# Kernel optimization log

Hardware: AMD Instinct MI355X
Metric: run time of the kernel (lower is better)

The kernel has to match this reference:

```python
import jax, jax.numpy as jnp
import numpy as np

# Static config matching init_kwargs / input_specs
IN_CH = 256
PATCH = 64
LAYERS = 4
B, H, W = 4, 256, 256
IC = IN_CH // 4        # SelfAttention inner channels (reduce=4)
C16 = IN_CH // 16      # f_test conv output channels
ALPHA = 0.05


def conv1x1(x, w, b):
    # x: (b,c,h,w), w: (out,c), b: (out,)  == nn.Conv2d(c,out,1)
    return jnp.einsum('bchw,oc->bohw', x, w) + b[None, :, None, None]


def setup_inputs() -> dict:
    key = jax.random.key(0)
    ks = jax.random.split(key, 12)
    s = 0.05
    return {
        'x':  jax.random.normal(ks[0], (B, IN_CH, H, W), jnp.float32),
        'Wq': jax.random.normal(ks[1], (IC, IN_CH), jnp.float32) * s,
        'bq': jax.random.normal(ks[2], (IC,), jnp.float32) * s,
        'Wk': jax.random.normal(ks[3], (IC, IN_CH), jnp.float32) * s,
        'bk': jax.random.normal(ks[4], (IC,), jnp.float32) * s,
        'Wv': jax.random.normal(ks[5], (IC, IN_CH), jnp.float32) * s,
        'bv': jax.random.normal(ks[6], (IC,), jnp.float32) * s,
        'Wr': jax.random.normal(ks[7], (IN_CH, IC), jnp.float32) * s,
        'br': jax.random.normal(ks[8], (IN_CH,), jnp.float32) * s,
        'Wf': jax.random.normal(ks[9], (C16, IN_CH), jnp.float32) * s,
        'bf': jax.random.normal(ks[10], (C16,), jnp.float32) * s,
    }


def reference(x, Wq, bq, Wk, bk, Wv, bv, Wr, br, Wf, bf):
    b, c, h, w = x.shape
    p = PATCH
    nh = h // p
    ic = IC

    # f_test applies the same 1x1 conv to the FULL image every call; its output
    # is identical each time, so precompute the per-(batch,channel) mean/var once.
    # torch uses .detach() -> stop_gradient.
    y2 = jax.lax.stop_gradient(conv1x1(x, Wf, bf))           # (b, C16, h, w)
    m2 = y2.mean(axis=(2, 3))                                 # (b, C16)
    v2 = y2.var(axis=(2, 3))                                  # biased var
    n1 = float(p * p)
    n2 = float(h * w)
    dfw = n1 + n2 - 2.0

    def ftest_decision(patch):
        # Two-group one-way ANOVA (scipy.stats.f_oneway) per (batch, channel).
        y1 = jax.lax.stop_gradient(conv1x1(patch, Wf, bf))    # (b, C16, p, p)
        m1 = y1.mean(axis=(2, 3))
        v1 = y1.var(axis=(2, 3))
        gm = (n1 * m1 + n2 * m2) / (n1 + n2)
        ssb = n1 * (m1 - gm) ** 2 + n2 * (m2 - gm) ** 2       # df_between = 1
        ssw = n1 * v1 + n2 * v2                               # sum sq dev within
        Fst = ssb / (ssw / dfw)
        # p-value = sf of F(1, dfw) = I_{dfw/(dfw+F)}(dfw/2, 1/2)
        pval = jax.scipy.special.betainc(dfw / 2.0, 0.5, dfw / (dfw + Fst))
        counts = jnp.sum(pval < ALPHA)
        return counts * 2 >= m1.size                          # scalar bool

    def attn(patch):
        # SelfAttention.forward: channel-to-channel attention over a patch.
        Q = conv1x1(patch, Wq, bq).reshape(b, ic, p * p)      # (b, ic, pp)
        # NOTE: original does K_pro.view(b, -1, inner_ch) -- a raw reshape,
        # NOT a transpose; we reproduce that exactly.
        K = conv1x1(patch, Wk, bk).reshape(b, p * p, ic)      # (b, pp, ic)
        V = conv1x1(patch, Wv, bv).reshape(b, ic, p * p)
        wts = jax.nn.softmax(jnp.einsum('bim,bmj->bij', Q, K), axis=1)  # (b,ic,ic)
        att = jnp.einsum('bij,bjm->bim', wts, V).reshape(b, ic, p, p)
        return conv1x1(att, Wr, br) + patch

    def run_patch(patch):
        # layer loop with data-dependent early break, expressed via masking
        stopped = jnp.array(False)
        for _ in range(LAYERS):
            stopped = stopped | ftest_decision(patch)  # break BEFORE attention
            patch = jnp.where(stopped, patch, attn(patch))
        return patch

    # Extract all nh*nh patches: (n_patches, b, c, p, p)
    patches = (x.reshape(b, c, nh, p, nh, p)
                .transpose(2, 4, 0, 1, 3, 5)
                .reshape(nh * nh, b, c, p, p))
    out_patches = jax.vmap(run_patch)(patches)

    # Faithful to original bug: x1 = x.clone() happens inside the patch loop,
    # so only the LAST patch's update survives in the returned tensor.
    x1 = x.at[:, :, (nh - 1) * p:, (nh - 1) * p:].set(out_patches[-1])
    return x1
```

## Files before the change

kernel.cpp:

```cpp
#include <hip/hip_runtime.h>

#define FCRIT 3.8415923532

#define OFF_FULL   0u
#define OFF_PATCH  1024u
#define OFF_S      8192u
#define OFF_Y3     1048576u
#define OFF_XH     16777216u
#define OFF_WH     41943040u
#define STATS_ZERO_BYTES 270336u

typedef __attribute__((ext_vector_type(8))) short short8;
typedef __attribute__((ext_vector_type(8))) unsigned short us8;
typedef __attribute__((ext_vector_type(4))) float f32x4;

static __device__ __forceinline__ double wred(double v) {
#pragma unroll
  for (int off = 32; off > 0; off >>= 1) v += __shfl_down(v, off, 64);
  return v;
}

static __device__ __forceinline__ unsigned short f2bf(float f) {
  union { float f; unsigned u; } v; v.f = f;
  unsigned r = v.u + 0x7fffu + ((v.u >> 16) & 1u);
  return (unsigned short)(r >> 16);
}
static __device__ __forceinline__ float bf2f(unsigned short h) {
  union { unsigned u; float f; } v; v.u = ((unsigned)h) << 16;
  return v.f;
}

static __device__ __forceinline__ bool is_stopped(const double* __restrict__ fullS,
                                                  const double* __restrict__ patchS,
                                                  int upto) {
  const int k = threadIdx.x & 63;
  const double fs = fullS[2 * k], fq = fullS[2 * k + 1];
  const double m2 = fs * (1.0 / 65536.0);
  const double v2 = fq * (1.0 / 65536.0) - m2 * m2;
  bool stopped = false;
  for (int l = 0; l <= upto; ++l) {
    const double* ps = patchS + (size_t)l * 128;
    const double s1 = ps[2 * k], s2 = ps[2 * k + 1];
    const double m1 = s1 * (1.0 / 4096.0);
    const double v1 = s2 * (1.0 / 4096.0) - m1 * m1;
    const double gm = (4096.0 * m1 + 65536.0 * m2) * (1.0 / 69632.0);
    const double d1 = m1 - gm, d2 = m2 - gm;
    const double ssb = 4096.0 * d1 * d1 + 65536.0 * d2 * d2;
    const double ssw = 4096.0 * v1 + 65536.0 * v2;
    const double F = ssb * (69630.0 / ssw);
    const unsigned long long bal = __ballot(F > FCRIT);
    const int cnt = __popcll(bal);
    stopped = stopped || (2 * cnt >= 64);
  }
  return stopped;
}

static __device__ __forceinline__ void fma16(float acc[4][4], float4 w, float4 v) {
  const float wa[4] = {w.x, w.y, w.z, w.w};
  const float va[4] = {v.x, v.y, v.z, v.w};
#pragma unroll
  for (int a = 0; a < 4; ++a)
#pragma unroll
    for (int c = 0; c < 4; ++c) acc[a][c] += wa[a] * va[c];
}

static __device__ __forceinline__ size_t pidx(int b, int c, int y, int x) {
  return (((size_t)b * 256 + c) * 256 + 192 + y) * 256 + 192 + x;
}

__global__ __launch_bounds__(256) void k_wcvt(const float* __restrict__ Wq,
                                              const float* __restrict__ Wk,
                                              const float* __restrict__ Wv,
                                              unsigned short* __restrict__ Whml) {
  const int idx0 = (blockIdx.x * 256 + threadIdx.x) * 4;
#pragma unroll
  for (int u = 0; u < 4; ++u) {
    const int i = idx0 + u;
    const int row = i >> 8, col = i & 255;
    const float v = (row < 64) ? Wq[row * 256 + col]
                  : (row < 128) ? Wk[(row - 64) * 256 + col]
                                : Wv[(row - 128) * 256 + col];
    const unsigned short h = f2bf(v);
    const float r1 = v - bf2f(h);
    const unsigned short m = f2bf(r1);
    const float r2 = r1 - bf2f(m);
    const unsigned short l = f2bf(r2);
    Whml[i] = h;
    Whml[49152 + i] = m;
    Whml[98304 + i] = l;
  }
}

__global__ __launch_bounds__(256) void k_main(const float* __restrict__ x,
                                              const float* __restrict__ Wf,
                                              const float* __restrict__ bf,
                                              float* __restrict__ out,
                                              double* __restrict__ fullS,
                                              double* __restrict__ patchS0) {
  __shared__ __align__(16) float WfT2[16 * 257];
  __shared__ __align__(16) float WfT[256 * 16];
  __shared__ double sm[4][16][2];
  __shared__ double sp[4][16][2];
  const int t = threadIdx.x;
  const int bb = blockIdx.x >> 7;
  const int rp = blockIdx.x & 127;

  for (int r = 0; r < 16; ++r) {
    int idx = r * 256 + t;
    WfT2[(idx >> 8) * 257 + (idx & 255)] = Wf[idx];
  }
  __syncthreads();
  for (int r = 0; r < 16; ++r) {
    int idx = r * 256 + t;
    int c = idx >> 4, o = idx & 15;
    WfT[c * 16 + o] = WfT2[o * 257 + c];
  }
  __syncthreads();

  const int r0 = rp * 2 + (t >> 7);
  const int col2 = (t & 127) * 2;
  const size_t base = (size_t)bb * 16777216 + (size_t)r0 * 256 + col2;
  const float* xp = x + base;
  float* op = out + base;
  const bool pStore = (rp >= 96) && ((t & 127) >= 96);

  float y0[16], y1[16];
#pragma unroll
  for (int o = 0; o < 16; ++o) { y0[o] = 0.f; y1[o] = 0.f; }

  for (int cb = 0; cb < 32; ++cb) {
    double v[8];
#pragma unroll
    for (int u = 0; u < 8; ++u)
      v[u] = *reinterpret_cast<const double*>(xp + (size_t)(cb * 8 + u) * 65536);
#pragma unroll
    for (int u = 0; u < 8; ++u) {
      double* dst = reinterpret_cast<double*>(op + (size_t)(cb * 8 + u) * 65536);
      if (pStore) *dst = v[u];
      else __builtin_nontemporal_store(v[u], dst);
      const int c = cb * 8 + u;
      float2 f = *reinterpret_cast<const float2*>(&v[u]);
      const float4* wf = reinterpret_cast<const float4*>(&WfT[c * 16]);
      const float4 w0 = wf[0], w1 = wf[1], w2 = wf[2], w3 = wf[3];
      const float wv[16] = {w0.x, w0.y, w0.z, w0.w, w1.x, w1.y, w1.z, w1.w,
                            w2.x, w2.y, w2.z, w2.w, w3.x, w3.y, w3.z, w3.w};
#pragma unroll
      for (int o = 0; o < 16; ++o) {
        y0[o] += wv[o] * f.x;
        y1[o] += wv[o] * f.y;
      }
    }
  }

  const int w = t >> 6, lane = t & 63;
  const bool pBlock = (rp >= 96);
  const bool pLane = ((t & 127) >= 96);
#pragma unroll 1
  for (int o = 0; o < 16; ++o) {
    const float bo = bf[o];
    const double a0 = (double)(y0[o] + bo), a1 = (double)(y1[o] + bo);
    double s1 = a0 + a1, s2 = a0 * a0 + a1 * a1;
    const double r1 = wred(s1), r2 = wred(s2);
    if (lane == 0) { sm[w][o][0] = r1; sm[w][o][1] = r2; }
    if (pBlock) {
      double p1 = pLane ? s1 : 0.0, p2 = pLane ? s2 : 0.0;
      p1 = wred(p1); p2 = wred(p2);
      if (lane == 0) { sp[w][o][0] = p1; sp[w][o][1] = p2; }
    }
  }
  __syncthreads();
  if (t < 32) {
    const int o = t >> 1, wh = t & 1;
    double s = sm[0][o][wh] + sm[1][o][wh] + sm[2][o][wh] + sm[3][o][wh];
    unsafeAtomicAdd(&fullS[(bb * 16 + o) * 2 + wh], s);
    if (pBlock) {
      double p = sp[0][o][wh] + sp[1][o][wh] + sp[2][o][wh] + sp[3][o][wh];
      unsafeAtomicAdd(&patchS0[(bb * 16 + o) * 2 + wh], p);
    }
  }
}

__global__ __launch_bounds__(256) void k_xcvt(const float* __restrict__ out,
                                              unsigned short* __restrict__ Xhml,
                                              const double* __restrict__ fullS,
                                              const double* __restrict__ patchS, int layer) {
  if (is_stopped(fullS, patchS, layer)) return;
  __shared__ float T[256 * 65];
  const int t = threadIdx.x;
  const int bb = blockIdx.x >> 6;
  const int y = blockIdx.x & 63;
  for (int r = 0; r < 64; ++r) {
    int idx = r * 256 + t;
    T[(idx >> 6) * 65 + (idx & 63)] = out[pidx(bb, idx >> 6, y, idx & 63)];
  }
  __syncthreads();
  const int px = t >> 2, c0 = (t & 3) * 64;
  const size_t dstbase = ((size_t)bb * 4096 + y * 64 + px) * 256 + c0;
#pragma unroll 1
  for (int g = 0; g < 8; ++g) {
    us8 hv, mv, lv;
#pragma unroll
    for (int j = 0; j < 8; ++j) {
      const float v = T[(c0 + g * 8 + j) * 65 + px];
      const unsigned short h = f2bf(v);
      const float r1 = v - bf2f(h);
      const unsigned short m = f2bf(r1);
      const float r2 = r1 - bf2f(m);
      const unsigned short l = f2bf(r2);
      hv[j] = (unsigned short)h; mv[j] = m; lv[j] = l;
    }
    *reinterpret_cast<us8*>(Xhml + dstbase + g * 8) = hv;
    *reinterpret_cast<us8*>(Xhml + 4194304u + dstbase + g * 8) = mv;
    *reinterpret_cast<us8*>(Xhml + 8388608u + dstbase + g * 8) = lv;
  }
}

__global__ __launch_bounds__(256) void k_qkv(const unsigned short* __restrict__ Whml,
                                             const float* __restrict__ bq,
                                             const float* __restrict__ bk,
                                             const float* __restrict__ bv,
                                             const unsigned short* __restrict__ Xhml,
                                             float* __restrict__ Y3,
                                             const double* __restrict__ fullS,
                                             const double* __restrict__ patchS, int layer) {
  if (is_stopped(fullS, patchS, layer)) return;
  __shared__ __align__(16) unsigned short Al[3][64][40];
  __shared__ __align__(16) unsigned short Bl[3][128][40];
  const int t = threadIdx.x;
  const int nt = blockIdx.x & 31;
  const int mt = (blockIdx.x >> 5) % 3;
  const int bb = blockIdx.x / 96;
  const int w = t >> 6, lane = t & 63;
  const int lo16 = lane & 15, hi4 = lane >> 4;

  f32x4 acc[4][2];
#pragma unroll
  for (int mf = 0; mf < 4; ++mf)
#pragma unroll
    for (int nf = 0; nf < 2; ++nf) acc[mf][nf] = (f32x4)0.f;

  const unsigned short* Wbase = Whml + mt * 64 * 256;
  const unsigned short* Xbase = Xhml + ((size_t)bb * 4096 + nt * 128) * 256;
  const int am = t >> 2, ak = (t & 3) * 8;
  const int bpx = t >> 1, bkh = (t & 1) * 16;

  for (int kc = 0; kc < 8; ++kc) {
    const int k0 = kc * 32;
    __syncthreads();
#pragma unroll
    for (int lev = 0; lev < 3; ++lev) {
      const us8 va = *reinterpret_cast<const us8*>(Wbase + lev * 49152 + am * 256 + k0 + ak);
      *reinterpret_cast<us8*>(&Al[lev][am][ak]) = va;
      const unsigned short* s = Xbase + (size_t)lev * 4194304 + (size_t)bpx * 256 + k0 + bkh;
      const us8 v0 = *reinterpret_cast<const us8*>(s);
      const us8 v1 = *reinterpret_cast<const us8*>(s + 8);
      *reinterpret_cast<us8*>(&Bl[lev][bpx][bkh]) = v0;
      *reinterpret_cast<us8*>(&Bl[lev][bpx][bkh + 8]) = v1;
    }
    __syncthreads();

    short8 af[3][4], bfr[3][2];
    const int koff = hi4 * 8;
#pragma unroll
    for (int lev = 0; lev < 3; ++lev) {
#pragma unroll
      for (int mf = 0; mf < 4; ++mf)
        af[lev][mf] = *reinterpret_cast<const short8*>(&Al[lev][mf * 16 + lo16][koff]);
#pragma unroll
      for (int nf = 0; nf < 2; ++nf)
        bfr[lev][nf] = *reinterpret_cast<const short8*>(&Bl[lev][w * 32 + nf * 16 + lo16][koff]);
    }
#pragma unroll
    for (int mf = 0; mf < 4; ++mf)
#pragma unroll
      for (int nf = 0; nf < 2; ++nf) {
        f32x4 c = acc[mf][nf];
        c = __builtin_amdgcn_mfma_f32_16x16x32_bf16(af[0][mf], bfr[0][nf], c, 0, 0, 0);
        c = __builtin_amdgcn_mfma_f32_16x16x32_bf16(af[0][mf], bfr[1][nf], c, 0, 0, 0);
        c = __builtin_amdgcn_mfma_f32_16x16x32_bf16(af[1][mf], bfr[0][nf], c, 0, 0, 0);
        c = __builtin_amdgcn_mfma_f32_16x16x32_bf16(af[0][mf], bfr[2][nf], c, 0, 0, 0);
        c = __builtin_amdgcn_mfma_f32_16x16x32_bf16(af[2][mf], bfr[0][nf], c, 0, 0, 0);
        c = __builtin_amdgcn_mfma_f32_16x16x32_bf16(af[1][mf], bfr[1][nf], c, 0, 0, 0);
        acc[mf][nf] = c;
      }
  }

  const float* bias = (mt == 0) ? bq : (mt == 1) ? bk : bv;
#pragma unroll
  for (int mf = 0; mf < 4; ++mf)
#pragma unroll
    for (int nf = 0; nf < 2; ++nf)
#pragma unroll
      for (int r = 0; r < 4; ++r) {
        const int mrow = mf * 16 + hi4 * 4 + r;
        const int col = nt * 128 + w * 32 + nf * 16 + lo16;
        Y3[((size_t)bb * 192 + mt * 64 + mrow) * 4096 + col] = acc[mf][nf][r] + bias[mrow];
      }
}

__global__ __launch_bounds__(256) void k_s(const float* __restrict__ Y3,
                                           float* __restrict__ Sbase,
                                           const double* __restrict__ fullS,
                                           const double* __restrict__ patchS, int layer) {
  if (is_stopped(fullS, patchS, layer)) return;
  __shared__ __align__(16) float QT[64][68];
  __shared__ __align__(16) float K2[64 * 64];
  const int t = threadIdx.x;
  const int mc = blockIdx.x & 63;
  const int bb = blockIdx.x >> 6;
  const int m0 = mc * 64;
  const float* Q = Y3 + (size_t)bb * 192 * 4096;
  const float* Kf = Q + 64 * 4096;
  for (int r = 0; r < 16; ++r) {
    int idx = r * 256 + t;
    int i = idx >> 6, ml = idx & 63;
    QT[ml][i] = Q[(size_t)i * 4096 + m0 + ml];
  }
  for (int r = 0; r < 16; ++r) {
    int idx = r * 256 + t;
    K2[idx] = Kf[(size_t)m0 * 64 + idx];
  }
  __syncthreads();
  const int tj = t & 15, ti = t >> 4;
  float acc[4][4] = {};
#pragma unroll 8
  for (int mm = 0; mm < 64; ++mm) {
    const float4 qv = *reinterpret_cast<const float4*>(&QT[mm][ti * 4]);
    const float4 kv = *reinterpret_cast<const float4*>(&K2[mm * 64 + tj * 4]);
    fma16(acc, qv, kv);
  }
  float* Sl = Sbase + (size_t)layer * 16384 + bb * 4096;
#pragma unroll
  for (int a = 0; a < 4; ++a)
#pragma unroll
    for (int c = 0; c < 4; ++c)
      unsafeAtomicAdd(&Sl[(ti * 4 + a) * 64 + tj * 4 + c], acc[a][c]);
}

__global__ __launch_bounds__(256) void k_awr(const float* __restrict__ Y3,
                                             const float* __restrict__ Sbase,
                                             const float* __restrict__ Wr,
                                             const float* __restrict__ br,
                                             float* __restrict__ out,
                                             const double* __restrict__ fullS,
                                             const double* __restrict__ patchS, int layer) {
  if (is_stopped(fullS, patchS, layer)) return;
  __shared__ __align__(16) float Sw[64 * 68];
  __shared__ __align__(16) float AV[64 * 68];
  __shared__ __align__(16) float WrF[128 * 65];
  const int t = threadIdx.x;
  const int y = blockIdx.x & 63;
  const int oh = (blockIdx.x >> 6) & 1;
  const int bb = blockIdx.x >> 7;

  const float* Vp = Y3 + (size_t)bb * 192 * 4096 + (size_t)128 * 4096 + y * 64;
  for (int r = 0; r < 16; ++r) {
    int idx = r * 256 + t;
    int j = idx >> 6, xx = idx & 63;
    AV[j * 68 + xx] = Vp[(size_t)j * 4096 + xx];
  }
  const float* Sl = Sbase + (size_t)layer * 16384 + bb * 4096;
  for (int r = 0; r < 16; ++r) {
    int idx = r * 256 + t;
    Sw[(idx & 63) * 68 + (idx >> 6)] = Sl[idx];
  }
  for (int r = 0; r < 32; ++r) {
    int idx = r * 256 + t;
    int ol = idx >> 6, i = idx & 63;
    WrF[ol * 65 + i] = Wr[(oh * 128 + ol) * 64 + i];
  }
  __syncthreads();

  if (t < 64) {
    float* colp = &Sw[t * 68];
    float mx = -1e30f;
#pragma unroll
    for (int i = 0; i < 64; ++i) mx = fmaxf(mx, colp[i]);
    float sum = 0.f;
#pragma unroll
    for (int i = 0; i < 64; ++i) {
      float e = __expf(colp[i] - mx);
      colp[i] = e;
      sum += e;
    }
    const float inv = 1.f / sum;
#pragma unroll
    for (int i = 0; i < 64; ++i) colp[i] *= inv;
  }
  __syncthreads();

  {
    const int ti = t >> 4, tx = t & 15;
    float acc[4][4] = {};
#pragma unroll 8
    for (int j = 0; j < 64; ++j) {
      const float4 wv = *reinterpret_cast<const float4*>(&Sw[j * 68 + ti * 4]);
      const float4 vv = *reinterpret_cast<const float4*>(&AV[j * 68 + tx * 4]);
      fma16(acc, wv, vv);
    }
    __syncthreads();
#pragma unroll
    for (int a = 0; a < 4; ++a) {
      float4 res;
      res.x = acc[a][0]; res.y = acc[a][1]; res.z = acc[a][2]; res.w = acc[a][3];
      *reinterpret_cast<float4*>(&AV[(ti * 4 + a) * 68 + tx * 4]) = res;
    }
  }
  __syncthreads();

  const int to = t >> 3, tx8 = t & 7;
  float acc[4][8] = {};
#pragma unroll 4
  for (int i = 0; i < 64; ++i) {
    const float4 a0 = *reinterpret_cast<const float4*>(&AV[i * 68 + tx8 * 8]);
    const float4 a1 = *reinterpret_cast<const float4*>(&AV[i * 68 + tx8 * 8 + 4]);
    const float av[8] = {a0.x, a0.y, a0.z, a0.w, a1.x, a1.y, a1.z, a1.w};
#pragma unroll
    for (int a = 0; a < 4; ++a) {
      const float wv = WrF[(to * 4 + a) * 65 + i];
#pragma unroll
      for (int c = 0; c < 8; ++c) acc[a][c] += wv * av[c];
    }
  }
#pragma unroll
  for (int a = 0; a < 4; ++a) {
    const int o = oh * 128 + to * 4 + a;
    const float bro = br[o];
    float* p = out + pidx(bb, o, y, tx8 * 8);
    float4 p0 = *reinterpret_cast<const float4*>(p);
    float4 p1 = *reinterpret_cast<const float4*>(p + 4);
    p0.x += acc[a][0] + bro; p0.y += acc[a][1] + bro;
    p0.z += acc[a][2] + bro; p0.w += acc[a][3] + bro;
    p1.x += acc[a][4] + bro; p1.y += acc[a][5] + bro;
    p1.z += acc[a][6] + bro; p1.w += acc[a][7] + bro;
    *reinterpret_cast<float4*>(p) = p0;
    *reinterpret_cast<float4*>(p + 4) = p1;
  }
}

__global__ __launch_bounds__(256) void k_ftest(const float* __restrict__ out,
                                               const float* __restrict__ Wf,
                                               const float* __restrict__ bf,
                                               double* __restrict__ patchS,
                                               const double* __restrict__ fullS, int layer) {
  if (is_stopped(fullS, patchS, layer)) return;
  __shared__ __align__(16) float WfT2[16 * 257];
  __shared__ __align__(16) float WfT[256 * 16];
  __shared__ float part[2 * 128 * 17];
  __shared__ double red[16][16][2];
  const int t = threadIdx.x;
  const int bb = blockIdx.x >> 5;
  const int rg = blockIdx.x & 31;

  for (int r = 0; r < 16; ++r) {
    int idx = r * 256 + t;
    WfT2[(idx >> 8) * 257 + (idx & 255)] = Wf[idx];
  }
  __syncthreads();
  for (int r = 0; r < 16; ++r) {
    int idx = r * 256 + t;
    int c = idx >> 4, o = idx & 15;
    WfT[c * 16 + o] = WfT2[o * 257 + c];
  }
  __syncthreads();

  const int h = t >> 7;
  const int px = t & 127;
  const int row = 192 + rg * 2 + (px >> 6);
  const int col = 192 + (px & 63);
  const size_t base = (size_t)bb * 16777216 + (size_t)h * 128 * 65536 + (size_t)row * 256 + col;

  float y[16] = {};
  for (int cb = 0; cb < 16; ++cb) {
    float v[8];
#pragma unroll
    for (int u = 0; u < 8; ++u)
      v[u] = out[base + (size_t)(cb * 8 + u) * 65536];
#pragma unroll
    for (int u = 0; u < 8; ++u) {
      const int c = h * 128 + cb * 8 + u;
      const float4* wf = reinterpret_cast<const float4*>(&WfT[c * 16]);
      const float4 w0 = wf[0], w1 = wf[1], w2 = wf[2], w3 = wf[3];
      const float wv[16] = {w0.x, w0.y, w0.z, w0.w, w1.x, w1.y, w1.z, w1.w,
                            w2.x, w2.y, w2.z, w2.w, w3.x, w3.y, w3.z, w3.w};
#pragma unroll
      for (int o = 0; o < 16; ++o) y[o] += wv[o] * v[u];
    }
  }
#pragma unroll
  for (int o = 0; o < 16; ++o) part[(h * 128 + px) * 17 + o] = y[o];
  __syncthreads();

  const int oo = t & 15, pxg = t >> 4;
  double s1 = 0.0, s2 = 0.0;
  const float bo = bf[oo];
#pragma unroll
  for (int j = 0; j < 8; ++j) {
    const int p = pxg * 8 + j;
    const float yv = part[p * 17 + oo] + part[(128 + p) * 17 + oo] + bo;
    const double v = (double)yv;
    s1 += v;
    s2 += v * v;
  }
  red[oo][pxg][0] = s1;
  red[oo][pxg][1] = s2;
  __syncthreads();
  if (t < 32) {
    const int o = t >> 1, wh = t & 1;
    double s = 0.0;
#pragma unroll
    for (int g = 0; g < 16; ++g) s += red[o][g][wh];
    unsafeAtomicAdd(&patchS[(size_t)(layer + 1) * 128 + (bb * 16 + o) * 2 + wh], s);
  }
}

extern "C" void kernel_launch(void* const* d_in, const int* in_sizes, int n_in,
                              void* d_out, int out_size, void* d_ws, size_t ws_size,
                              hipStream_t stream) {
  const float* x  = (const float*)d_in[0];
  const float* Wq = (const float*)d_in[1];
  const float* bq = (const float*)d_in[2];
  const float* Wk = (const float*)d_in[3];
  const float* bk = (const float*)d_in[4];
  const float* Wv = (const float*)d_in[5];
  const float* bv = (const float*)d_in[6];
  const float* Wr = (const float*)d_in[7];
  const float* br = (const float*)d_in[8];
  const float* Wf = (const float*)d_in[9];
  const float* bf = (const float*)d_in[10];
  float* out = (float*)d_out;
  char* ws = (char*)d_ws;

  double* fullS  = (double*)(ws + OFF_FULL);
  double* patchS = (double*)(ws + OFF_PATCH);
  float* Sb = (float*)(ws + OFF_S);
  float* Y3 = (float*)(ws + OFF_Y3);
  unsigned short* Xhml = (unsigned short*)(ws + OFF_XH);
  unsigned short* Whml = (unsigned short*)(ws + OFF_WH);

  (void)hipMemsetAsync(ws, 0, STATS_ZERO_BYTES, stream);
  k_wcvt<<<48, 256, 0, stream>>>(Wq, Wk, Wv, Whml);
  k_main<<<512, 256, 0, stream>>>(x, Wf, bf, out, fullS, patchS);
  for (int l = 0; l < 4; ++l) {
    k_xcvt<<<256, 256, 0, stream>>>(out, Xhml, fullS, patchS, l);
    k_qkv<<<384, 256, 0, stream>>>(Whml, bq, bk, bv, Xhml, Y3, fullS, patchS, l);
    k_s<<<256, 256, 0, stream>>>(Y3, Sb, fullS, patchS, l);
    k_awr<<<512, 256, 0, stream>>>(Y3, Sb, Wr, br, out, fullS, patchS, l);
    if (l < 3) k_ftest<<<128, 256, 0, stream>>>(out, Wf, bf, patchS, fullS, l);
  }
}
```

Baseline: 252.4 us.

## Compute all layers speculatively, fuse bf16 split into producers, select result at end

Drops the per-kernel stop checks and computes all four attention layers unconditionally. Each layer's result goes to a pixel-major buffer, and a final selection kernel copies the correct layer's output into the image based on the F-test decisions. The separate conversion kernel is removed: the hi/mid bf16 split is fused into k_main and k_awr, and the QKV GEMM drops the third precision level for X (5 MFMAs instead of 6). This removes a launch per layer and a transpose pass, at the cost of always doing all layers and slightly lower precision on activations.

```diff
diff --git a/kernel.cpp b/kernel.cpp
--- a/kernel.cpp
+++ b/kernel.cpp
@@ -1,24 +1,21 @@
 #include <hip/hip_runtime.h>
+
+typedef __attribute__((ext_vector_type(8))) short short8;
+typedef __attribute__((ext_vector_type(8))) unsigned short us8;
+typedef __attribute__((ext_vector_type(4))) float f32x4;
 
 #define FCRIT 3.8415923532
 
 #define OFF_FULL   0u
 #define OFF_PATCH  1024u
 #define OFF_S      8192u
+#define ZERO_BYTES 270336u
 #define OFF_Y3     1048576u
 #define OFF_XH     16777216u
 #define OFF_WH     41943040u
-#define STATS_ZERO_BYTES 270336u
-
-typedef __attribute__((ext_vector_type(8))) short short8;
-typedef __attribute__((ext_vector_type(8))) unsigned short us8;
-typedef __attribute__((ext_vector_type(4))) float f32x4;
-
-static __device__ __forceinline__ double wred(double v) {
-#pragma unroll
-  for (int off = 32; off > 0; off >>= 1) v += __shfl_down(v, off, 64);
-  return v;
-}
+#define OFF_PB     50331648u
+
+#define MFMA __builtin_amdgcn_mfma_f32_16x16x32_bf16
 
 static __device__ __forceinline__ unsigned short f2bf(float f) {
   union { float f; unsigned u; } v; v.f = f;
@@ -29,43 +26,13 @@
   union { unsigned u; float f; } v; v.u = ((unsigned)h) << 16;
   return v.f;
 }
-
-static __device__ __forceinline__ bool is_stopped(const double* __restrict__ fullS,
-                                                  const double* __restrict__ patchS,
-                                                  int upto) {
-  const int k = threadIdx.x & 63;
-  const double fs = fullS[2 * k], fq = fullS[2 * k + 1];
-  const double m2 = fs * (1.0 / 65536.0);
-  const double v2 = fq * (1.0 / 65536.0) - m2 * m2;
-  bool stopped = false;
-  for (int l = 0; l <= upto; ++l) {
-    const double* ps = patchS + (size_t)l * 128;
-    const double s1 = ps[2 * k], s2 = ps[2 * k + 1];
-    const double m1 = s1 * (1.0 / 4096.0);
-    const double v1 = s2 * (1.0 / 4096.0) - m1 * m1;
-    const double gm = (4096.0 * m1 + 65536.0 * m2) * (1.0 / 69632.0);
-    const double d1 = m1 - gm, d2 = m2 - gm;
-    const double ssb = 4096.0 * d1 * d1 + 65536.0 * d2 * d2;
-    const double ssw = 4096.0 * v1 + 65536.0 * v2;
-    const double F = ssb * (69630.0 / ssw);
-    const unsigned long long bal = __ballot(F > FCRIT);
-    const int cnt = __popcll(bal);
-    stopped = stopped || (2 * cnt >= 64);
-  }
-  return stopped;
-}
-
-static __device__ __forceinline__ void fma16(float acc[4][4], float4 w, float4 v) {
-  const float wa[4] = {w.x, w.y, w.z, w.w};
-  const float va[4] = {v.x, v.y, v.z, v.w};
-#pragma unroll
-  for (int a = 0; a < 4; ++a)
-#pragma unroll
-    for (int c = 0; c < 4; ++c) acc[a][c] += wa[a] * va[c];
-}
-
-static __device__ __forceinline__ size_t pidx(int b, int c, int y, int x) {
-  return (((size_t)b * 256 + c) * 256 + 192 + y) * 256 + 192 + x;
+static __device__ __forceinline__ void split2(float v, unsigned short& h, unsigned short& m) {
+  h = f2bf(v); float r = v - bf2f(h); m = f2bf(r);
+}
+static __device__ __forceinline__ double wred(double v) {
+#pragma unroll
+  for (int off = 32; off > 0; off >>= 1) v += __shfl_down(v, off, 64);
+  return v;
 }
 
 __global__ __launch_bounds__(256) void k_wcvt(const float* __restrict__ Wq,
@@ -84,10 +51,9 @@
     const float r1 = v - bf2f(h);
     const unsigned short m = f2bf(r1);
     const float r2 = r1 - bf2f(m);
-    const unsigned short l = f2bf(r2);
     Whml[i] = h;
     Whml[49152 + i] = m;
-    Whml[98304 + i] = l;
+    Whml[98304 + i] = f2bf(r2);
   }
 }
 
@@ -96,7 +62,8 @@
                                               const float* __restrict__ bf,
                                               float* __restrict__ out,
                                               double* __restrict__ fullS,
-                                              double* __restrict__ patchS0) {
+                                              double* __restrict__ patchS0,
+                                              unsigned short* __restrict__ XB) {
   __shared__ __align__(16) float WfT2[16 * 257];
   __shared__ __align__(16) float WfT[256 * 16];
   __shared__ double sm[4][16][2];
@@ -123,6 +90,11 @@
   const float* xp = x + base;
   float* op = out + base;
   const bool pStore = (rp >= 96) && ((t & 127) >= 96);
+  size_t xbbase = 0;
+  if (pStore) {
+    const int py = r0 - 192, pxc = col2 - 192;
+    xbbase = ((size_t)bb * 4096 + py * 64 + pxc) * 256;
+  }
 
   float y0[16], y1[16];
 #pragma unroll
@@ -133,6 +105,7 @@
 #pragma unroll
     for (int u = 0; u < 8; ++u)
       v[u] = *reinterpret_cast<const double*>(xp + (size_t)(cb * 8 + u) * 65536);
+    us8 h0, h1, m0, m1;
 #pragma unroll
     for (int u = 0; u < 8; ++u) {
       double* dst = reinterpret_cast<double*>(op + (size_t)(cb * 8 + u) * 65536);
@@ -140,6 +113,11 @@
       else __builtin_nontemporal_store(v[u], dst);
       const int c = cb * 8 + u;
       float2 f = *reinterpret_cast<const float2*>(&v[u]);
+      if (pStore) {
+        unsigned short hh, mm;
+        split2(f.x, hh, mm); h0[u] = hh; m0[u] = mm;
+        split2(f.y, hh, mm); h1[u] = hh; m1[u] = mm;
+      }
       const float4* wf = reinterpret_cast<const float4*>(&WfT[c * 16]);
       const float4 w0 = wf[0], w1 = wf[1], w2 = wf[2], w3 = wf[3];
       const float wv[16] = {w0.x, w0.y, w0.z, w0.w, w1.x, w1.y, w1.z, w1.w,
@@ -149,6 +127,12 @@
         y0[o] += wv[o] * f.x;
         y1[o] += wv[o] * f.y;
       }
+    }
+    if (pStore) {
+      *(us8*)(XB + xbbase + cb * 8) = h0;
+      *(us8*)(XB + 4194304u + xbbase + cb * 8) = m0;
+      *(us8*)(XB + xbbase + 256 + cb * 8) = h1;
+      *(us8*)(XB + 4194304u + xbbase + 256 + cb * 8) = m1;
     }
   }
 
@@ -180,52 +164,14 @@
   }
 }
 
-__global__ __launch_bounds__(256) void k_xcvt(const float* __restrict__ out,
-                                              unsigned short* __restrict__ Xhml,
-                                              const double* __restrict__ fullS,
-                                              const double* __restrict__ patchS, int layer) {
-  if (is_stopped(fullS, patchS, layer)) return;
-  __shared__ float T[256 * 65];
-  const int t = threadIdx.x;
-  const int bb = blockIdx.x >> 6;
-  const int y = blockIdx.x & 63;
-  for (int r = 0; r < 64; ++r) {
-    int idx = r * 256 + t;
-    T[(idx >> 6) * 65 + (idx & 63)] = out[pidx(bb, idx >> 6, y, idx & 63)];
-  }
-  __syncthreads();
-  const int px = t >> 2, c0 = (t & 3) * 64;
-  const size_t dstbase = ((size_t)bb * 4096 + y * 64 + px) * 256 + c0;
-#pragma unroll 1
-  for (int g = 0; g < 8; ++g) {
-    us8 hv, mv, lv;
-#pragma unroll
-    for (int j = 0; j < 8; ++j) {
-      const float v = T[(c0 + g * 8 + j) * 65 + px];
-      const unsigned short h = f2bf(v);
-      const float r1 = v - bf2f(h);
-      const unsigned short m = f2bf(r1);
-      const float r2 = r1 - bf2f(m);
-      const unsigned short l = f2bf(r2);
-      hv[j] = (unsigned short)h; mv[j] = m; lv[j] = l;
-    }
-    *reinterpret_cast<us8*>(Xhml + dstbase + g * 8) = hv;
-    *reinterpret_cast<us8*>(Xhml + 4194304u + dstbase + g * 8) = mv;
-    *reinterpret_cast<us8*>(Xhml + 8388608u + dstbase + g * 8) = lv;
-  }
-}
-
 __global__ __launch_bounds__(256) void k_qkv(const unsigned short* __restrict__ Whml,
                                              const float* __restrict__ bq,
                                              const float* __restrict__ bk,
                                              const float* __restrict__ bv,
                                              const unsigned short* __restrict__ Xhml,
-                                             float* __restrict__ Y3,
-                                             const double* __restrict__ fullS,
-                                             const double* __restrict__ patchS, int layer) {
-  if (is_stopped(fullS, patchS, layer)) return;
+                                             float* __restrict__ Y3) {
   __shared__ __align__(16) unsigned short Al[3][64][40];
-  __shared__ __align__(16) unsigned short Bl[3][128][40];
+  __shared__ __align__(16) unsigned short Bl[2][128][40];
   const int t = threadIdx.x;
   const int nt = blockIdx.x & 31;
   const int mt = (blockIdx.x >> 5) % 3;
@@ -251,6 +197,9 @@
     for (int lev = 0; lev < 3; ++lev) {
       const us8 va = *reinterpret_cast<const us8*>(Wbase + lev * 49152 + am * 256 + k0 + ak);
       *reinterpret_cast<us8*>(&Al[lev][am][ak]) = va;
+    }
+#pragma unroll
+    for (int lev = 0; lev < 2; ++lev) {
       const unsigned short* s = Xbase + (size_t)lev * 4194304 + (size_t)bpx * 256 + k0 + bkh;
       const us8 v0 = *reinterpret_cast<const us8*>(s);
       const us8 v1 = *reinterpret_cast<const us8*>(s + 8);
@@ -259,28 +208,28 @@
     }
     __syncthreads();
 
-    short8 af[3][4], bfr[3][2];
+    short8 af[3][4], bfr[2][2];
     const int koff = hi4 * 8;
 #pragma unroll
-    for (int lev = 0; lev < 3; ++lev) {
+    for (int lev = 0; lev < 3; ++lev)
 #pragma unroll
       for (int mf = 0; mf < 4; ++mf)
         af[lev][mf] = *reinterpret_cast<const short8*>(&Al[lev][mf * 16 + lo16][koff]);
 #pragma unroll
+    for (int lev = 0; lev < 2; ++lev)
+#pragma unroll
       for (int nf = 0; nf < 2; ++nf)
         bfr[lev][nf] = *reinterpret_cast<const short8*>(&Bl[lev][w * 32 + nf * 16 + lo16][koff]);
-    }
 #pragma unroll
     for (int mf = 0; mf < 4; ++mf)
 #pragma unroll
       for (int nf = 0; nf < 2; ++nf) {
         f32x4 c = acc[mf][nf];
-        c = __builtin_amdgcn_mfma_f32_16x16x32_bf16(af[0][mf], bfr[0][nf], c, 0, 0, 0);
-        c = __builtin_amdgcn_mfma_f32_16x16x32_bf16(af[0][mf], bfr[1][nf], c, 0, 0, 0);
-        c = __builtin_amdgcn_mfma_f32_16x16x32_bf16(af[1][mf], bfr[0][nf], c, 0, 0, 0);
-        c = __builtin_amdgcn_mfma_f32_16x16x32_bf16(af[0][mf], bfr[2][nf], c, 0, 0, 0);
-        c = __builtin_amdgcn_mfma_f32_16x16x32_bf16(af[2][mf], bfr[0][nf], c, 0, 0, 0);
-        c = __builtin_amdgcn_mfma_f32_16x16x32_bf16(af[1][mf], bfr[1][nf], c, 0, 0, 0);
+        c = MFMA(af[0][mf], bfr[0][nf], c, 0, 0, 0);
+        c = MFMA(af[0][mf], bfr[1][nf], c, 0, 0, 0);
+        c = MFMA(af[1][mf], bfr[0][nf], c, 0, 0, 0);
+        c = MFMA(af[1][mf], bfr[1][nf], c, 0, 0, 0);
+        c = MFMA(af[2][mf], bfr[0][nf], c, 0, 0, 0);
         acc[mf][nf] = c;
       }
   }
@@ -299,10 +248,7 @@
 }
 
 __global__ __launch_bounds__(256) void k_s(const float* __restrict__ Y3,
-                                           float* __restrict__ Sbase,
-                                           const double* __restrict__ fullS,
-                                           const double* __restrict__ patchS, int layer) {
-  if (is_stopped(fullS, patchS, layer)) return;
+                                           float* __restrict__ Sbase, int layer) {
   __shared__ __align__(16) float QT[64][68];
   __shared__ __align__(16) float K2[64 * 64];
   const int t = threadIdx.x;
@@ -327,7 +273,12 @@
   for (int mm = 0; mm < 64; ++mm) {
     const float4 qv = *reinterpret_cast<const float4*>(&QT[mm][ti * 4]);
     const float4 kv = *reinterpret_cast<const float4*>(&K2[mm * 64 + tj * 4]);
-    fma16(acc, qv, kv);
+    const float qa[4] = {qv.x, qv.y, qv.z, qv.w};
+    const float ka[4] = {kv.x, kv.y, kv.z, kv.w};
+#pragma unroll
+    for (int a = 0; a < 4; ++a)
+#pragma unroll
+      for (int c = 0; c < 4; ++c) acc[a][c] += qa[a] * ka[c];
   }
   float* Sl = Sbase + (size_t)layer * 16384 + bb * 4096;
 #pragma unroll
@@ -341,10 +292,9 @@
                                              const float* __restrict__ Sbase,
                                              const float* __restrict__ Wr,
                                              const float* __restrict__ br,
-                                             float* __restrict__ out,
-                                             const double* __restrict__ fullS,
-                                             const double* __restrict__ patchS, int layer) {
-  if (is_stopped(fullS, patchS, layer)) return;
+                                             const float* __restrict__ out,
+                                             float* __restrict__ PB,
+                                             unsigned short* __restrict__ XB, int layer) {
   __shared__ __align__(16) float Sw[64 * 68];
   __shared__ __align__(16) float AV[64 * 68];
   __shared__ __align__(16) float WrF[128 * 65];
@@ -396,7 +346,12 @@
     for (int j = 0; j < 64; ++j) {
       const float4 wv = *reinterpret_cast<const float4*>(&Sw[j * 68 + ti * 4]);
       const float4 vv = *reinterpret_cast<const float4*>(&AV[j * 68 + tx * 4]);
-      fma16(acc, wv, vv);
+      const float wa[4] = {wv.x, wv.y, wv.z, wv.w};
+      const float va[4] = {vv.x, vv.y, vv.z, vv.w};
+#pragma unroll
+      for (int a = 0; a < 4; ++a)
+#pragma unroll
+        for (int c = 0; c < 4; ++c) acc[a][c] += wa[a] * va[c];
     }
     __syncthreads();
 #pragma unroll
@@ -422,35 +377,72 @@
       for (int c = 0; c < 8; ++c) acc[a][c] += wv * av[c];
     }
   }
+  __syncthreads();
+
+  float* PLT = WrF;
 #pragma unroll
   for (int a = 0; a < 4; ++a) {
-    const int o = oh * 128 + to * 4 + a;
-    const float bro = br[o];
-    float* p = out + pidx(bb, o, y, tx8 * 8);
-    float4 p0 = *reinterpret_cast<const float4*>(p);
-    float4 p1 = *reinterpret_cast<const float4*>(p + 4);
-    p0.x += acc[a][0] + bro; p0.y += acc[a][1] + bro;
-    p0.z += acc[a][2] + bro; p0.w += acc[a][3] + bro;
-    p1.x += acc[a][4] + bro; p1.y += acc[a][5] + bro;
-    p1.z += acc[a][6] + bro; p1.w += acc[a][7] + bro;
-    *reinterpret_cast<float4*>(p) = p0;
-    *reinterpret_cast<float4*>(p + 4) = p1;
-  }
-}
-
-__global__ __launch_bounds__(256) void k_ftest(const float* __restrict__ out,
+    const float bro = br[oh * 128 + to * 4 + a];
+#pragma unroll
+    for (int c = 0; c < 8; ++c)
+      PLT[(tx8 * 8 + c) * 130 + to * 4 + a] = acc[a][c] + bro;
+  }
+  __syncthreads();
+
+  const int px = t >> 2, cq = t & 3;
+  const size_t rowIdx = ((size_t)bb * 4096 + y * 64 + px) * 256 + oh * 128 + cq * 32;
+  float vals[32];
+  if (layer == 0) {
+    const size_t ob = ((size_t)bb * 256 + oh * 128 + cq * 32) * 65536
+                    + (size_t)(192 + y) * 256 + 192 + px;
+#pragma unroll
+    for (int j = 0; j < 32; ++j)
+      vals[j] = PLT[px * 130 + cq * 32 + j] + out[ob + (size_t)j * 65536];
+  } else {
+    const float* pp = PB + (size_t)(layer - 1) * 4194304 + rowIdx;
+#pragma unroll
+    for (int u = 0; u < 8; ++u) {
+      const float4 pv = *reinterpret_cast<const float4*>(pp + u * 4);
+      vals[u * 4 + 0] = PLT[px * 130 + cq * 32 + u * 4 + 0] + pv.x;
+      vals[u * 4 + 1] = PLT[px * 130 + cq * 32 + u * 4 + 1] + pv.y;
+      vals[u * 4 + 2] = PLT[px * 130 + cq * 32 + u * 4 + 2] + pv.z;
+      vals[u * 4 + 3] = PLT[px * 130 + cq * 32 + u * 4 + 3] + pv.w;
+    }
+  }
+  float* dstP = PB + (size_t)layer * 4194304 + rowIdx;
+#pragma unroll
+  for (int u = 0; u < 8; ++u) {
+    float4 fv;
+    fv.x = vals[u * 4 + 0]; fv.y = vals[u * 4 + 1];
+    fv.z = vals[u * 4 + 2]; fv.w = vals[u * 4 + 3];
+    *reinterpret_cast<float4*>(dstP + u * 4) = fv;
+  }
+  if (layer < 3) {
+#pragma unroll
+    for (int g = 0; g < 4; ++g) {
+      us8 hv, mv;
+#pragma unroll
+      for (int j = 0; j < 8; ++j) {
+        unsigned short h, m;
+        split2(vals[g * 8 + j], h, m);
+        hv[j] = h; mv[j] = m;
+      }
+      *(us8*)(XB + rowIdx + g * 8) = hv;
+      *(us8*)(XB + 4194304u + rowIdx + g * 8) = mv;
+    }
+  }
+}
+
+__global__ __launch_bounds__(256) void k_ftest(const float* __restrict__ PB,
                                                const float* __restrict__ Wf,
                                                const float* __restrict__ bf,
-                                               double* __restrict__ patchS,
-                                               const double* __restrict__ fullS, int layer) {
-  if (is_stopped(fullS, patchS, layer)) return;
+                                               double* __restrict__ patchS, int layer) {
   __shared__ __align__(16) float WfT2[16 * 257];
-  __shared__ __align__(16) float WfT[256 * 16];
-  __shared__ float part[2 * 128 * 17];
-  __shared__ double red[16][16][2];
+  __shared__ __align__(16) float WfT[4096];
+  __shared__ float part[256 * 17];
+  __shared__ double red[512];
   const int t = threadIdx.x;
-  const int bb = blockIdx.x >> 5;
-  const int rg = blockIdx.x & 31;
+  const int bb = blockIdx.x >> 6, y = blockIdx.x & 63;
 
   for (int r = 0; r < 16; ++r) {
     int idx = r * 256 + t;
@@ -464,53 +456,101 @@
   }
   __syncthreads();
 
-  const int h = t >> 7;
-  const int px = t & 127;
-  const int row = 192 + rg * 2 + (px >> 6);
-  const int col = 192 + (px & 63);
-  const size_t base = (size_t)bb * 16777216 + (size_t)h * 128 * 65536 + (size_t)row * 256 + col;
-
-  float y[16] = {};
-  for (int cb = 0; cb < 16; ++cb) {
-    float v[8];
-#pragma unroll
-    for (int u = 0; u < 8; ++u)
-      v[u] = out[base + (size_t)(cb * 8 + u) * 65536];
-#pragma unroll
-    for (int u = 0; u < 8; ++u) {
-      const int c = h * 128 + cb * 8 + u;
-      const float4* wf = reinterpret_cast<const float4*>(&WfT[c * 16]);
-      const float4 w0 = wf[0], w1 = wf[1], w2 = wf[2], w3 = wf[3];
-      const float wv[16] = {w0.x, w0.y, w0.z, w0.w, w1.x, w1.y, w1.z, w1.w,
-                            w2.x, w2.y, w2.z, w2.w, w3.x, w3.y, w3.z, w3.w};
-#pragma unroll
-      for (int o = 0; o < 16; ++o) y[o] += wv[o] * v[u];
-    }
-  }
-#pragma unroll
-  for (int o = 0; o < 16; ++o) part[(h * 128 + px) * 17 + o] = y[o];
+  const int px = t & 63, cg = t >> 6;
+  const float* src = PB + (size_t)layer * 4194304
+                   + ((size_t)bb * 4096 + y * 64 + px) * 256 + cg * 64;
+  float po[16] = {};
+#pragma unroll 4
+  for (int u = 0; u < 16; ++u) {
+    const float4 v = *reinterpret_cast<const float4*>(src + u * 4);
+    const float va[4] = {v.x, v.y, v.z, v.w};
+#pragma unroll
+    for (int k = 0; k < 4; ++k) {
+      const float* wc = &WfT[(cg * 64 + u * 4 + k) * 16];
+#pragma unroll
+      for (int o = 0; o < 16; ++o) po[o] += wc[o] * va[k];
+    }
+  }
+#pragma unroll
+  for (int o = 0; o < 16; ++o) part[(cg * 64 + px) * 17 + o] = po[o];
   __syncthreads();
 
   const int oo = t & 15, pxg = t >> 4;
   double s1 = 0.0, s2 = 0.0;
   const float bo = bf[oo];
 #pragma unroll
-  for (int j = 0; j < 8; ++j) {
-    const int p = pxg * 8 + j;
-    const float yv = part[p * 17 + oo] + part[(128 + p) * 17 + oo] + bo;
-    const double v = (double)yv;
-    s1 += v;
-    s2 += v * v;
-  }
-  red[oo][pxg][0] = s1;
-  red[oo][pxg][1] = s2;
+  for (int j = 0; j < 4; ++j) {
+    const int p = pxg * 4 + j;
+    const float yv = part[p * 17 + oo] + part[(64 + p) * 17 + oo]
+                   + part[(128 + p) * 17 + oo] + part[(192 + p) * 17 + oo] + bo;
+    const double vd = (double)yv;
+    s1 += vd; s2 += vd * vd;
+  }
+  red[(oo * 16 + pxg) * 2] = s1;
+  red[(oo * 16 + pxg) * 2 + 1] = s2;
   __syncthreads();
   if (t < 32) {
     const int o = t >> 1, wh = t & 1;
     double s = 0.0;
 #pragma unroll
-    for (int g = 0; g < 16; ++g) s += red[o][g][wh];
+    for (int g = 0; g < 16; ++g) s += red[(o * 16 + g) * 2 + wh];
     unsafeAtomicAdd(&patchS[(size_t)(layer + 1) * 128 + (bb * 16 + o) * 2 + wh], s);
+  }
+}
+
+__global__ __launch_bounds__(256) void k_sel(float* __restrict__ out, char* __restrict__ ws) {
+  __shared__ __align__(16) float T[64 * 68];
+  const double* fullS  = (const double*)(ws + OFF_FULL);
+  const double* patchS = (const double*)(ws + OFF_PATCH);
+  const float* PB = (const float*)(ws + OFF_PB);
+  const int t = threadIdx.x;
+  const int b2 = blockIdx.x >> 6, y = blockIdx.x & 63;
+  const int lane = t & 63;
+
+  int jsel = 4;
+  {
+    const int k = lane;
+    const double fs = fullS[2 * k], fq = fullS[2 * k + 1];
+    const double m2 = fs * (1.0 / 65536.0);
+    const double v2 = fq * (1.0 / 65536.0) - m2 * m2;
+#pragma unroll
+    for (int l = 0; l < 4; ++l) {
+      const double* ps = patchS + (size_t)l * 128;
+      const double s1 = ps[2 * k], s2 = ps[2 * k + 1];
+      const double m1 = s1 * (1.0 / 4096.0);
+      const double v1 = s2 * (1.0 / 4096.0) - m1 * m1;
+      const double gm = (4096.0 * m1 + 65536.0 * m2) * (1.0 / 69632.0);
+      const double d1 = m1 - gm, d2 = m2 - gm;
+      const double ssb = 4096.0 * d1 * d1 + 65536.0 * d2 * d2;
+      const double ssw = 4096.0 * v1 + 65536.0 * v2;
+      const double F = ssb * (69630.0 / ssw);
+      const unsigned long long bal = __ballot(F > FCRIT);
+      if (2 * __popcll(bal) >= 64 && jsel == 4) jsel = l;
+    }
+  }
+  if (jsel == 0) return;
+  const float* src = PB + (size_t)(jsel - 1) * 4194304;
+  for (int oc = 0; oc < 4; ++oc) {
+    __syncthreads();
+    { const int pxl = t >> 2, og = (t & 3) * 16;
+#pragma unroll
+      for (int u = 0; u < 4; ++u) {
+        const float4 v = *reinterpret_cast<const float4*>(src + ((size_t)b2 * 4096 + y * 64 + pxl) * 256
+                                                          + oc * 64 + og + u * 4);
+        *reinterpret_cast<float4*>(&T[pxl * 68 + og + u * 4]) = v;
+      } }
+    __syncthreads();
+    { const int ol = t & 63, pg = t >> 6;
+      float* op = out + (((size_t)b2 * 256 + oc * 64 + ol) * 256 + 192 + y) * 256 + 192 + pg * 16;
+#pragma unroll
+      for (int u4 = 0; u4 < 4; ++u4) {
+        float4 v;
+        v.x = T[(pg * 16 + u4 * 4 + 0) * 68 + ol];
+        v.y = T[(pg * 16 + u4 * 4 + 1) * 68 + ol];
+        v.z = T[(pg * 16 + u4 * 4 + 2) * 68 + ol];
+        v.w = T[(pg * 16 + u4 * 4 + 3) * 68 + ol];
+        *reinterpret_cast<float4*>(op + u4 * 4) = v;
+      } }
   }
 }
 
@@ -535,17 +575,18 @@
   double* patchS = (double*)(ws + OFF_PATCH);
   float* Sb = (float*)(ws + OFF_S);
   float* Y3 = (float*)(ws + OFF_Y3);
-  unsigned short* Xhml = (unsigned short*)(ws + OFF_XH);
+  unsigned short* XB = (unsigned short*)(ws + OFF_XH);
   unsigned short* Whml = (unsigned short*)(ws + OFF_WH);
-
-  (void)hipMemsetAsync(ws, 0, STATS_ZERO_BYTES, stream);
+  float* PB = (float*)(ws + OFF_PB);
+
+  (void)hipMemsetAsync(ws, 0, ZERO_BYTES, stream);
   k_wcvt<<<48, 256, 0, stream>>>(Wq, Wk, Wv, Whml);
-  k_main<<<512, 256, 0, stream>>>(x, Wf, bf, out, fullS, patchS);
+  k_main<<<512, 256, 0, stream>>>(x, Wf, bf, out, fullS, patchS, XB);
   for (int l = 0; l < 4; ++l) {
-    k_xcvt<<<256, 256, 0, stream>>>(out, Xhml, fullS, patchS, l);
-    k_qkv<<<384, 256, 0, stream>>>(Whml, bq, bk, bv, Xhml, Y3, fullS, patchS, l);
-    k_s<<<256, 256, 0, stream>>>(Y3, Sb, fullS, patchS, l);
-    k_awr<<<512, 256, 0, stream>>>(Y3, Sb, Wr, br, out, fullS, patchS, l);
-    if (l < 3) k_ftest<<<128, 256, 0, stream>>>(out, Wf, bf, patchS, fullS, l);
-  }
-}
+    k_qkv<<<384, 256, 0, stream>>>(Whml, bq, bk, bv, XB, Y3);
+    k_s<<<256, 256, 0, stream>>>(Y3, Sb, l);
+    k_awr<<<512, 256, 0, stream>>>(Y3, Sb, Wr, br, out, PB, XB, l);
+    if (l < 3) k_ftest<<<256, 256, 0, stream>>>(PB, Wf, bf, patchS, l);
+  }
+  k_sel<<<256, 256, 0, stream>>>(out, ws);
+}
```

Result: slower. 461.7 us (+82.9%).
